# Performance work log

Hardware: AMD Instinct MI355X
Metric: run time of the kernel (lower is better)

## Reference

```python
import jax, jax.numpy as jnp
import numpy as np
from jax import lax

B, TZ, TT = 16, 2048, 512
D, DFF, L, V, HEADS = 256, 1024, 6, 512, 4
CH, HID, K, FLOWS, G = 256, 256, 5, 4, 256
PAD_ID = 0
NEG = -1e9
SCALE = 0.02


def setup_inputs():
    key = jax.random.key(0)
    ks = jax.random.split(key, 20)
    n = lambda i, shape, s=SCALE: jax.random.normal(ks[i], shape, jnp.float32) * s
    return {
        'z': jax.random.normal(ks[0], (B, TZ, CH), jnp.float32),
        'text': jax.random.randint(ks[1], (B, TT), 1, V),  # low=1 so no pad tokens
        'cond': jax.random.normal(ks[2], (B, G), jnp.float32),
        'embed': n(3, (V, D), 1.0),
        'wq': n(4, (L, D, D)), 'wk': n(5, (L, D, D)), 'wv': n(6, (L, D, D)), 'wo': n(7, (L, D, D)),
        'bq': jnp.zeros((L, D)), 'bk': jnp.zeros((L, D)), 'bv': jnp.zeros((L, D)), 'bo': jnp.zeros((L, D)),
        'ln1_g': jnp.ones((L, D)), 'ln1_b': jnp.zeros((L, D)),
        'ln2_g': jnp.ones((L, D)), 'ln2_b': jnp.zeros((L, D)),
        'w1': n(8, (L, D, DFF)), 'b1': jnp.zeros((L, DFF)),
        'w2': n(9, (L, DFF, D)), 'b2': jnp.zeros((L, D)),
        'mu_w': n(10, (D, D)), 'mu_b': jnp.zeros((D,)),
        'lv_w': n(11, (D, D)), 'lv_b': jnp.zeros((D,)),
        'flow_in': n(12, (FLOWS, CH // 2, HID)), 'flow_in_b': jnp.zeros((FLOWS, HID)),
        'flow_cond': n(13, (FLOWS, G, HID)),
        'flow_conv': n(14, (FLOWS, K, HID, HID)), 'flow_conv_b': jnp.zeros((FLOWS, HID)),
        'flow_out': n(15, (FLOWS, HID, CH // 2)), 'flow_out_b': jnp.zeros((FLOWS, CH // 2)),
    }


def _pos_encoding(length, d):
    pos = np.arange(length)[:, None].astype(np.float32)
    i = np.arange(d)[None, :]
    angle = pos / np.power(10000.0, (2 * (i // 2)) / d)
    pe = np.where(i % 2 == 0, np.sin(angle), np.cos(angle))
    return jnp.asarray(pe, jnp.float32)


def _ln(x, g, b):
    m = jnp.mean(x, -1, keepdims=True)
    v = jnp.var(x, -1, keepdims=True)
    return g * (x - m) * lax.rsqrt(v + 1e-6) + b


def _mha(x, wq, wk, wv, wo, bq, bk, bv, bo, bias):
    Bq, T, _ = x.shape
    dh = D // HEADS
    heads = lambda y: y.reshape(Bq, T, HEADS, dh).transpose(0, 2, 1, 3)
    q, k, v = heads(x @ wq + bq), heads(x @ wk + bk), heads(x @ wv + bv)
    scores = jnp.einsum('bhqd,bhkd->bhqk', q, k) / jnp.sqrt(jnp.float32(dh)) + bias
    attn = jax.nn.softmax(scores, axis=-1)
    out = jnp.einsum('bhqk,bhkd->bhqd', attn, v).transpose(0, 2, 1, 3).reshape(Bq, T, D)
    return out @ wo + bo


def _mas_path(logp, text_mask):
    # Viterbi monotonic alignment: each latent frame t maps to text index j(t),
    # j nondecreasing with steps in {0, 1}, start at 0, end at last valid token.
    Bq, Tz, Tt = logp.shape
    Q0 = jnp.where(jnp.arange(Tt) == 0, logp[:, 0, :], NEG)

    def fwd(Q, lt):
        Qs = jnp.concatenate([jnp.full((Bq, 1), NEG, Q.dtype), Q[:, :-1]], axis=1)
        return lt + jnp.maximum(Q, Qs), Qs > Q  # choice True => came from j-1

    _, choices = lax.scan(fwd, Q0, jnp.swapaxes(logp, 0, 1)[1:])  # [Tz-1,B,Tt]
    j_last = jnp.sum(text_mask, axis=1).astype(jnp.int32) - 1

    def bwd(j, ch):
        c = jnp.take_along_axis(ch, j[:, None], axis=1)[:, 0]
        jp = j - c.astype(jnp.int32)
        return jp, jp

    _, path_rev = lax.scan(bwd, j_last, choices[::-1])
    path = jnp.concatenate([path_rev[::-1], j_last[None]], axis=0)  # [Tz,B]
    return jnp.swapaxes(path, 0, 1)


def _forward(z, text, cond, embed, wq, wk, wv, wo, bq, bk, bv, bo, ln1_g, ln1_b, ln2_g, ln2_b,
             w1, b1, w2, b2, mu_w, mu_b, lv_w, lv_b,
             flow_in, flow_in_b, flow_cond, flow_conv, flow_conv_b, flow_out, flow_out_b):
    text_mask = text != PAD_ID  # [B,TT]
    bias = jnp.where(text_mask[:, None, None, :], 0.0, NEG)
    # text encoder: scaled embedding + sinusoidal PE + post-LN transformer blocks
    h = embed[text] * jnp.sqrt(jnp.float32(D)) + _pos_encoding(TT, D)[None]
    for l in range(L):
        h = _ln(h + _mha(h, wq[l], wk[l], wv[l], wo[l], bq[l], bk[l], bv[l], bo[l], bias), ln1_g[l], ln1_b[l])
        ffn = jax.nn.relu(h @ w1[l] + b1[l]) @ w2[l] + b2[l]
        h = _ln(h + ffn, ln2_g[l], ln2_b[l])
    mu = h @ mu_w + mu_b
    logvar = h @ lv_w + lv_b
    # residual coupling flows (mean-only, conditioned on global vector)
    zc = z
    for f in range(FLOWS):
        x0, x1 = jnp.split(zc, 2, axis=-1)
        hh = x0 @ flow_in[f] + flow_in_b[f] + (cond @ flow_cond[f])[:, None, :]
        hh = jnp.tanh(lax.conv_general_dilated(hh, flow_conv[f], (1,), 'SAME', rhs_dilation=(1,),
                                               dimension_numbers=('NWC', 'WIO', 'NWC')) + flow_conv_b[f])
        m = hh @ flow_out[f] + flow_out_b[f]
        zc = jnp.concatenate([x1 + m, x0], axis=-1)  # coupling + flip
    # gaussian log-likelihood between latent frames and text distributions
    spr = jnp.exp(-logvar)  # [B,TT,D]
    nc1 = jnp.sum(-0.5 * jnp.log(2.0 * jnp.pi) - 0.5 * logvar, axis=-1)  # [B,TT]
    nc2 = jnp.einsum('btd,bjd->btj', -0.5 * zc * zc, spr)
    nc3 = jnp.einsum('btd,bjd->btj', zc, mu * spr)
    nc4 = jnp.sum(-0.5 * mu * mu * spr, axis=-1)  # [B,TT]
    logp = nc1[:, None, :] + nc2 + nc3 + nc4[:, None, :]  # [B,TZ,TT]
    logp = jnp.where(text_mask[:, None, :], logp, NEG)
    path = _mas_path(logp, text_mask)  # [B,TZ] int32
    ctx = mu[jnp.arange(B)[:, None], path]  # expand text mu along latent time
    return ctx, h


def reference(z, text, cond, embed, wq, wk, wv, wo, bq, bk, bv, bo, ln1_g, ln1_b, ln2_g, ln2_b,
              w1, b1, w2, b2, mu_w, mu_b, lv_w, lv_b,
              flow_in, flow_in_b, flow_cond, flow_conv, flow_conv_b, flow_out, flow_out_b):
    return _forward(z, text, cond, embed, wq, wk, wv, wo, bq, bk, bv, bo, ln1_g, ln1_b, ln2_g, ln2_b,
                    w1, b1, w2, b2, mu_w, mu_b, lv_w, lv_b,
                    flow_in, flow_in_b, flow_cond, flow_conv, flow_conv_b, flow_out, flow_out_b)
```

## Files before the change

### kernel.cpp

```cpp
#include <hip/hip_runtime.h>

#define BB 16
#define TZ_ 2048
#define TT_ 512
#define D_ 256
#define DFF_ 1024
#define L_ 6
#define HEADS_ 4
#define DH_ 64
#define CH_ 256
#define HID_ 256
#define KCV 5
#define FLOWS_ 4
#define G_ 256
#define NEGF (-1000000000.0f)
#define LOG2PI 1.8378770664093453f

typedef unsigned short u16;
typedef __attribute__((ext_vector_type(8))) short short8v;
typedef __attribute__((ext_vector_type(4))) float f32x4;

__device__ __forceinline__ float wsum(float v){
#pragma unroll
  for (int o = 32; o; o >>= 1) v += __shfl_xor(v, o);
// ... 81 lines not shown
#pragma unroll
  for (int c=0;c<16;c+=4){
    float4 v = *(const float4*)(inb + (size_t)(kt + r)*istride + nt + cq + c);
    td[r][cq+c+0]=v.x; td[r][cq+c+1]=v.y; td[r][cq+c+2]=v.z; td[r][cq+c+3]=v.w;
  }
  __syncthreads();
#pragma unroll
  for (int c=0;c<16;c+=4){
    float4 v = make_float4(td[cq+c+0][r], td[cq+c+1][r], td[cq+c+2][r], td[cq+c+3][r]);
    *(float4*)(outb + (size_t)(nt + r)*ostride + kt + cq + c) = v;
  }
}

__global__ __launch_bounds__(256) void k_vt(const float* __restrict__ QKV, float* __restrict__ VT){
  __shared__ float td[64][65];
  const int b = blockIdx.z, dt = blockIdx.x, jt = blockIdx.y, t = threadIdx.x;
  const float* inb = QKV + (size_t)b*512*768 + 512;
  float* outb = VT + (size_t)b*131072;
  const int r = t>>2, cq = (t&3)*16;
#pragma unroll
  for (int c=0;c<16;c+=4){
    float4 v = *(const float4*)(inb + (size_t)(jt*64 + r)*768 + dt*64 + cq + c);
    td[r][cq+c+0]=v.x; td[r][cq+c+1]=v.y; td[r][cq+c+2]=v.z; td[r][cq+c+3]=v.w;
  }
  __syncthreads();
#pragma unroll
  for (int c=0;c<16;c+=4){
    float4 v = make_float4(td[cq+c+0][r], td[cq+c+1][r], td[cq+c+2][r], td[cq+c+3][r]);
    *(float4*)(outb + (size_t)(dt*64 + r)*512 + jt*64 + cq + c) = v;
  }
}

__global__ void k_bcat(const float* __restrict__ bq, const float* __restrict__ bk,
                       const float* __restrict__ bv, const float* __restrict__ mu_b,
                       const float* __restrict__ lv_b,
                       float* __restrict__ BQKV, float* __restrict__ MULVB){
  int i = blockIdx.x*256 + threadIdx.x;
  if (i < 4608){
    int l = i/768, c = i%768;
    float v = c<256 ? bq[l*256+c] : (c<512 ? bk[l*256+c-256] : bv[l*256+c-512]);
    BQKV[i] = v;
  } else if (i < 5120){
    int c = i-4608;
    MULVB[c] = c<256 ? mu_b[c] : lv_b[c-256];
  }
}

template<int WN, int EPI, int AM, int BMD>
__global__ __launch_bounds__(256,2) void k_mg(
  const void* __restrict__ Ap, const void* __restrict__ ApL, int lda, int azhi, int azlo,
  const void* __restrict__ Bp, const void* __restrict__ BpL, int ldb, int bzhi, int bzlo,
  const float* __restrict__ bias, const int* __restrict__ text,
  const float* __restrict__ nc1v, const float* __restrict__ nc4v,
  float* __restrict__ C, int ldc, int czhi, int czlo, int K)
{
  constexpr int BN = WN*32;
  __shared__ u16 AH[4096], AL[4096];
  __shared__ u16 BH[BN*32], BL[BN*32];
  char* AHB=(char*)AH; char* ALB=(char*)AL; char* BHB=(char*)BH; char* BLB=(char*)BL;
  const int t = threadIdx.x, z = blockIdx.z;
  const int m0 = blockIdx.y*128, n0 = blockIdx.x*BN;
  const size_t aoff = (size_t)(z>>2)*azhi + (size_t)(z&3)*azlo;
  const size_t boff = (size_t)(z>>2)*bzhi + (size_t)(z&3)*bzlo;
  const size_t coff = (size_t)(z>>2)*czhi + (size_t)(z&3)*czlo;
  const int w = t>>6, l = t&63;
  const int wr = (w>>1)*64, wc = (w&1)*(WN*16);
  const int lr = l&15, lg = l>>4;
  const int srow = t>>1, sseg = t&1;
  const int q  = (srow>>1)&3;
  const int wo0 = srow*64 + ((((sseg<<1)|0)^q)<<4);
  const int wo1 = srow*64 + ((((sseg<<1)|1)^q)<<4);
  const bool bact = (WN==4) || (t < 128);
  const int qa = ((wr+lr)>>1)&3, qb2 = ((wc+lr)>>1)&3;
  const int raBase = (wr+lr)*64 + ((lg^qa)<<4);
  const int rbBase = (wc+lr)*64 + ((lg^qb2)<<4);

  const float* Af = nullptr; const u16* AfH = nullptr; const u16* AfL = nullptr;
  if constexpr (AM==0 || AM==2){ Af = (const float*)Ap + aoff; }
  else { AfH = (const u16*)Ap + aoff; AfL = (const u16*)ApL + aoff; }
  const float* Bf = nullptr; const u16* BfH = nullptr; const u16* BfL = nullptr;
  if constexpr (BMD==0){ Bf = (const float*)Bp + boff; }
  else { BfH = (const u16*)Bp + boff; BfL = (const u16*)BpL + boff; }

  f32x4 acc[4][WN];
#pragma unroll
  for (int i=0;i<4;i++)
#pragma unroll
    for (int j=0;j<WN;j++) acc[i][j] = (f32x4){0.f,0.f,0.f,0.f};

  for (int k0 = 0; k0 < K; k0 += 32){
    uint4 ahi0, ahi1, alo0, alo1;
    if constexpr (AM==0){
      const float* p = Af + (size_t)(m0+srow)*lda + k0 + sseg*16;
      float4 a0=*(const float4*)p, a1=*(const float4*)(p+4);
      float4 a2=*(const float4*)(p+8), a3=*(const float4*)(p+12);
      cvt8t(a0,a1,ahi0,alo0); cvt8t(a2,a3,ahi1,alo1);
    } else if constexpr (AM==1){
      const u16* ph = AfH + (size_t)(m0+srow)*lda + k0 + sseg*16;
      const u16* pl = AfL + (size_t)(m0+srow)*lda + k0 + sseg*16;
      ahi0 = *(const uint4*)ph; ahi1 = *(const uint4*)(ph+8);
      alo0 = *(const uint4*)pl; alo1 = *(const uint4*)(pl+8);
    } else {
      int kg = k0 + sseg*16;
      const float* p = Af + (size_t)(m0+srow)*lda + (kg < 256 ? kg : kg - 256);
      float4 a0=*(const float4*)p, a1=*(const float4*)(p+4);
      float4 a2=*(const float4*)(p+8), a3=*(const float4*)(p+12);
      if (kg >= 256){
        a0.x=-0.5f*a0.x*a0.x; a0.y=-0.5f*a0.y*a0.y; a0.z=-0.5f*a0.z*a0.z; a0.w=-0.5f*a0.w*a0.w;
        a1.x=-0.5f*a1.x*a1.x; a1.y=-0.5f*a1.y*a1.y; a1.z=-0.5f*a1.z*a1.z; a1.w=-0.5f*a1.w*a1.w;
        a2.x=-0.5f*a2.x*a2.x; a2.y=-0.5f*a2.y*a2.y; a2.z=-0.5f*a2.z*a2.z; a2.w=-0.5f*a2.w*a2.w;
        a3.x=-0.5f*a3.x*a3.x; a3.y=-0.5f*a3.y*a3.y; a3.z=-0.5f*a3.z*a3.z; a3.w=-0.5f*a3.w*a3.w;
      }
      cvt8r(a0,a1,ahi0,alo0); cvt8r(a2,a3,ahi1,alo1);
    }
    uint4 bhi0, bhi1, blo0, blo1;
    if (bact){
      if constexpr (BMD==0){
        const float* p = Bf + (size_t)(n0+srow)*ldb + k0 + sseg*16;
        float4 b0=*(const float4*)p, b1=*(const float4*)(p+4);
        float4 b2=*(const float4*)(p+8), b3=*(const float4*)(p+12);
        cvt8t(b0,b1,bhi0,blo0); cvt8t(b2,b3,bhi1,blo1);
      } else {
        const u16* ph = BfH + (size_t)(n0+srow)*ldb + k0 + sseg*16;
        const u16* pl = BfL + (size_t)(n0+srow)*ldb + k0 + sseg*16;
        bhi0 = *(const uint4*)ph; bhi1 = *(const uint4*)(ph+8);
        blo0 = *(const uint4*)pl; blo1 = *(const uint4*)(pl+8);
      }
    }
    __syncthreads();
    *(uint4*)(AHB + wo0) = ahi0;  *(uint4*)(AHB + wo1) = ahi1;
    *(uint4*)(ALB + wo0) = alo0;  *(uint4*)(ALB + wo1) = alo1;
    if (bact){
      *(uint4*)(BHB + wo0) = bhi0;  *(uint4*)(BHB + wo1) = bhi1;
      *(uint4*)(BLB + wo0) = blo0;  *(uint4*)(BLB + wo1) = blo1;
    }
    __syncthreads();
    short8v fah[4], fal[4], fbh[WN], fbl[WN];
#pragma unroll
    for (int i=0;i<4;i++){
      fah[i] = *(short8v*)(AHB + raBase + i*1024);
      fal[i] = *(short8v*)(ALB + raBase + i*1024);
    }
#pragma unroll
    for (int j=0;j<WN;j++){
      fbh[j] = *(short8v*)(BHB + rbBase + j*1024);
      fbl[j] = *(short8v*)(BLB + rbBase + j*1024);
    }
#pragma unroll
    for (int i=0;i<4;i++)
#pragma unroll
      for (int j=0;j<WN;j++){
        acc[i][j] = __builtin_amdgcn_mfma_f32_16x16x32_bf16(fah[i], fbh[j], acc[i][j], 0,0,0);
        acc[i][j] = __builtin_amdgcn_mfma_f32_16x16x32_bf16(fal[i], fbh[j], acc[i][j], 0,0,0);
        acc[i][j] = __builtin_amdgcn_mfma_f32_16x16x32_bf16(fah[i], fbl[j], acc[i][j], 0,0,0);
      }
  }

#pragma unroll
  for (int i=0;i<4;i++){
    int mm0 = m0 + wr + i*16 + (lg<<2);
#pragma unroll
    for (int j=0;j<WN;j++){
      int nn = n0 + wc + j*16 + lr;
      float bs = 0.f; float ncb = 0.f; bool msk = true;
      if (EPI==0 || EPI==1) bs = bias ? bias[nn] : 0.f;
      if (EPI==2) msk = (text[(z>>2)*TT_ + nn] != 0);
      if (EPI==3){ ncb = nc1v[z*TT_+nn] + nc4v[z*TT_+nn]; msk = (text[z*TT_+nn] != 0); }
      f32x4 v = acc[i][j];
#pragma unroll
      for (int r=0;r<4;r++){
        int m = mm0 + r;
        float x;
        if (EPI==0)      x = v[r] + bs;
        else if (EPI==1) x = fmaxf(v[r] + bs, 0.f);
        else if (EPI==2) x = v[r]*0.125f + (msk ? 0.f : NEGF);
        else             x = msk ? (v[r] + ncb) : NEGF;
        C[coff + (size_t)m*ldc + nn] = x;
      }
    }
  }
}

__global__ __launch_bounds__(256) void k_softmax(float* __restrict__ S){
  size_t row = (size_t)blockIdx.x*4 + (threadIdx.x >> 6);
  float* p = S + row*TT_;
  int ln = threadIdx.x & 63;
  float4 a = *(float4*)(p + ln*8);
  float4 b = *(float4*)(p + ln*8 + 4);
  float x[8] = {a.x,a.y,a.z,a.w,b.x,b.y,b.z,b.w};
  float m = x[0];
#pragma unroll
  for (int i=1;i<8;i++) m = fmaxf(m, x[i]);
#pragma unroll
  for (int o2=32;o2;o2>>=1) m = fmaxf(m, __shfl_xor(m, o2));
  float s = 0.f;
#pragma unroll
  for (int i=0;i<8;i++){ x[i] = expf(x[i]-m); s += x[i]; }
  s = wsum(s);
  float inv = 1.0f/s;
  *(float4*)(p + ln*8)     = make_float4(x[0]*inv, x[1]*inv, x[2]*inv, x[3]*inv);
  *(float4*)(p + ln*8 + 4) = make_float4(x[4]*inv, x[5]*inv, x[6]*inv, x[7]*inv);
}

__global__ __launch_bounds__(256) void k_lnres(const float* __restrict__ y,
  const float* __restrict__ g, const float* __restrict__ bb, float* __restrict__ h){
  size_t row = blockIdx.x; int d = threadIdx.x;
  float v = h[row*D_ + d] + y[row*D_ + d];
  float s = wsum(v), s2 = wsum(v*v);
  __shared__ float r1[4], r2[4];
  int w = d >> 6;
  if ((d & 63) == 0){ r1[w] = s; r2[w] = s2; }
  __syncthreads();
  s  = r1[0]+r1[1]+r1[2]+r1[3];
  s2 = r2[0]+r2[1]+r2[2]+r2[3];
  float mean = s * (1.0f/D_);
  float var  = s2 * (1.0f/D_) - mean*mean;
  float inv  = rsqrtf(var + 1e-6f);
  h[row*D_ + d] = g[d]*(v - mean)*inv + bb[d];
// ... 38 lines not shown
    float wv2; u16 *dh, *dl; int idx;
    if (i < 32768){
      int n = i >> 7, k = i & 127;
      wv2 = win[k*256 + n]; dh = WITH; dl = WITL; idx = i;
    } else if (i < 360448){
      int jj = i - 32768;
      int o = jj / 1280, r = jj - o*1280;
      wv2 = wconv[(size_t)r*256 + o]; dh = WCTH; dl = WCTL; idx = jj;
    } else {
      int jj = i - 360448;
      int o = jj >> 8, k = jj & 255;
      wv2 = wout[k*128 + o]; dh = WOTH; dl = WOTL; idx = jj;
    }
    u16 hh = f2bf(wv2);
    dh[idx] = hh;
    dl[idx] = f2bf(wv2 - bf2f(hh));
  } else if (bid < 3584){
    size_t i = ((size_t)(bid-1536)*256 + t) << 3;
    size_t m2 = i >> 7; int k = (int)(i & 127);
    const float* src = zsrc + m2*256 + k;
    float4 a = *(const float4*)src; float4 b2 = *(const float4*)(src+4);
    float vv[8] = {a.x,a.y,a.z,a.w,b2.x,b2.y,b2.z,b2.w};
    short8v oh, ol;
#pragma unroll
    for (int r=0;r<8;r++){
      u16 hh = f2bf(vv[r]);
      oh[r] = (short)hh;
      ol[r] = (short)f2bf(vv[r] - bf2f(hh));
    }
    *(short8v*)(xh + i) = oh;
    *(short8v*)(xl + i) = ol;
  } else {
    int b = bid - 3584, n = t;
    float s = 0.f;
    for (int k2=0;k2<G_;k2++) s = fmaf(cond[b*G_ + k2], fcw[k2*HID_ + n], s);
    condp[b*HID_ + n] = s;
  }
}

__global__ void k_padzero2(u16* __restrict__ XpH, u16* __restrict__ XpL){
  int i = blockIdx.x*256 + threadIdx.x;
  u16* P = (i >> 14) ? XpL : XpH;
  int ii = i & 16383;
  int b = ii >> 10, rr = (ii >> 8) & 3, c = ii & 255;
  int row = (rr < 2) ? rr : (2048 + rr);
  P[((size_t)b*2052 + row)*256 + c] = 0;
}

template<int EPI, int SPLITOUT>
__global__ __launch_bounds__(256,2) void k_mf2(
  const u16* __restrict__ Ah, const u16* __restrict__ Al, int lda, int padA,
  const u16* __restrict__ Bh, const u16* __restrict__ Bl, int ldb,
  const float* __restrict__ bias, const float* __restrict__ cnd,
  void* __restrict__ CH, void* __restrict__ CL, int ldc, int padC, int K)
{
  __shared__ u16 AsmH[4096], AsmL[4096], BsmH[4096], BsmL[4096];
  char* AHB=(char*)AsmH; char* ALB=(char*)AsmL;
  char* BHB=(char*)BsmH; char* BLB=(char*)BsmL;
  const int t = threadIdx.x;
  const int m0 = blockIdx.y << 7, n0 = blockIdx.x << 7;
  const int w = t >> 6, l = t & 63;
  const int wr = (w >> 1) << 6, wc = (w & 1) << 6;
  const int lr = l & 15, lg = l >> 4;
  const int srow = t >> 1, sseg = t & 1;
  const int q = (srow >> 1) & 3;
  const int wo0 = srow*64 + ((((sseg<<1)|0) ^ q) << 4);
  const int wo1 = srow*64 + ((((sseg<<1)|1) ^ q) << 4);
  const int am = m0 + srow;
  const size_t aoff = (size_t)(am + padA*(am >> 11))*lda + (sseg << 4);
  const u16* AhP = Ah + aoff;
  const u16* AlP = Al + aoff;
  const size_t boff = (size_t)(n0 + srow)*ldb + (sseg << 4);
  const u16* BhP = Bh + boff;
  const u16* BlP = Bl + boff;
  const int qa = ((wr + lr) >> 1) & 3, qb = ((wc + lr) >> 1) & 3;
  const int raBase = (wr + lr)*64 + ((lg ^ qa) << 4);
  const int rbBase = (wc + lr)*64 + ((lg ^ qb) << 4);
  f32x4 acc[4][4];
#pragma unroll
  for (int i=0;i<4;i++)
#pragma unroll
    for (int j=0;j<4;j++) acc[i][j] = (f32x4){0.f,0.f,0.f,0.f};

  for (int k0 = 0; k0 < K; k0 += 32){
    float4 ah0 = *(const float4*)(AhP + k0);
    float4 ah1 = *(const float4*)(AhP + k0 + 8);
    float4 al0 = *(const float4*)(AlP + k0);
    float4 al1 = *(const float4*)(AlP + k0 + 8);
    float4 bh0 = *(const float4*)(BhP + k0);
    float4 bh1 = *(const float4*)(BhP + k0 + 8);
    float4 bl0 = *(const float4*)(BlP + k0);
    float4 bl1 = *(const float4*)(BlP + k0 + 8);
    __syncthreads();
    *(float4*)(AHB + wo0) = ah0;  *(float4*)(AHB + wo1) = ah1;
    *(float4*)(ALB + wo0) = al0;  *(float4*)(ALB + wo1) = al1;
    *(float4*)(BHB + wo0) = bh0;  *(float4*)(BHB + wo1) = bh1;
    *(float4*)(BLB + wo0) = bl0;  *(float4*)(BLB + wo1) = bl1;
    __syncthreads();
    short8v fah[4], fal[4], fbh[4], fbl[4];
#pragma unroll
    for (int i=0;i<4;i++){
      fah[i] = *(short8v*)(AHB + raBase + i*1024);
      fal[i] = *(short8v*)(ALB + raBase + i*1024);
    }
#pragma unroll
    for (int j=0;j<4;j++){
      fbh[j] = *(short8v*)(BHB + rbBase + j*1024);
      fbl[j] = *(short8v*)(BLB + rbBase + j*1024);
    }
#pragma unroll
    for (int i=0;i<4;i++)
#pragma unroll
      for (int j=0;j<4;j++){
        acc[i][j] = __builtin_amdgcn_mfma_f32_16x16x32_bf16(fah[i], fbh[j], acc[i][j], 0, 0, 0);
        acc[i][j] = __builtin_amdgcn_mfma_f32_16x16x32_bf16(fal[i], fbh[j], acc[i][j], 0, 0, 0);
        acc[i][j] = __builtin_amdgcn_mfma_f32_16x16x32_bf16(fah[i], fbl[j], acc[i][j], 0, 0, 0);
      }
  }

#pragma unroll
  for (int i=0;i<4;i++){
    int mbase = m0 + wr + i*16 + (lg << 2);
#pragma unroll
    for (int j=0;j<4;j++){
      int nn = n0 + wc + j*16 + lr;
      float bs = bias[nn];
      f32x4 v = acc[i][j];
#pragma unroll
      for (int r=0;r<4;r++){
        int m = mbase + r;
        float x = v[r] + bs;
        if (EPI == 1) x += cnd[((m >> 11) << 8) + nn];
        if (EPI == 2) x = tanhf(x);
        if (EPI == 3) x += cnd[(size_t)m*256 + 128 + nn];
        size_t ro = (size_t)(m + padC*(m >> 11))*ldc + nn;
        if (SPLITOUT){
          u16 xh = f2bf(x);
          ((u16*)CH)[ro] = xh;
          ((u16*)CL)[ro] = f2bf(x - bf2f(xh));
        } else {
          ((float*)CH)[ro] = x;
          if (EPI == 3)
            ((float*)CH)[(size_t)m*ldc + 128 + nn] = cnd[(size_t)m*256 + nn];
        }
      }
    }
  }
}

#define MCH 8
#define NCHK (TZ_/MCH)
__device__ __forceinline__ int swsl(int s){ return s ^ ((s>>3)&7); }

__device__ __forceinline__ void mas_row(float4 u0, float4 u1, float* Q, int ln, int tr,
                                        unsigned char* __restrict__ cb){
  if (tr == 0){
    if (ln == 0) Q[0] = u0.x;
    return;
  }
  float v[8] = {u0.x,u0.y,u0.z,u0.w,u1.x,u1.y,u1.z,u1.w};
  float qp = __shfl_up(Q[7], 1);
  if (ln == 0) qp = NEGF;
  unsigned bits = 0; float qs = qp;
#pragma unroll
  for (int i=0;i<8;i++){
    float old = Q[i];
    if (qs > old) bits |= (1u<<i);
    Q[i] = v[i] + fmaxf(old, qs);
    qs = old;
  }
  cb[(size_t)(tr-1)*64 + ln] = (unsigned char)bits;
}

__global__ __launch_bounds__(512) void k_mas(const float* __restrict__ lp,
  const int* __restrict__ text, unsigned char* __restrict__ cho, int* __restrict__ path)
{
  const int b = blockIdx.x, t = threadIdx.x, ln = t & 63;
  const float* L = lp + (size_t)b*TZ_*TT_;
  __shared__ float buf[3][MCH*TT_];
  __shared__ __align__(16) unsigned char lch[3][4096];
  const int frow = t >> 6, k64 = t & 63;
  const size_t gsrc = (size_t)frow*TT_ + k64*8;
  char* b0p = (char*)&buf[0][0];
  char* b1p = (char*)&buf[1][0];
  char* b2p = (char*)&buf[2][0];
  char* bufb[3] = {b0p, b1p, b2p};
  const int wroff = frow*2048;
  const int ws0 = wroff + (swsl(2*k64)<<4);
  const int ws1 = wroff + (swsl(2*k64+1)<<4);
  const int rs0 = swsl(2*ln)<<4;
  const int rs1 = swsl(2*ln+1)<<4;
  unsigned char* cb = cho + (size_t)b*TZ_*64;

  {
    float4 a0 = *(const float4*)(L + gsrc);
    float4 a1 = *(const float4*)(L + gsrc + 4);
    float4 c0 = *(const float4*)(L + (size_t)MCH*TT_ + gsrc);
    float4 c1 = *(const float4*)(L + (size_t)MCH*TT_ + gsrc + 4);
    *(float4*)(b0p + ws0) = a0;  *(float4*)(b0p + ws1) = a1;
    *(float4*)(b1p + ws0) = c0;  *(float4*)(b1p + ws1) = c1;
  }
  float4 pA0 = *(const float4*)(L + (size_t)2*MCH*TT_ + gsrc);
  float4 pA1 = *(const float4*)(L + (size_t)2*MCH*TT_ + gsrc + 4);
  float4 pB0 = *(const float4*)(L + (size_t)3*MCH*TT_ + gsrc);
  float4 pB1 = *(const float4*)(L + (size_t)3*MCH*TT_ + gsrc + 4);
  __syncthreads();

  float Q[8];
#pragma unroll
  for (int i=0;i<8;i++) Q[i] = NEGF;
  float4 hA0,hA1,hA2,hA3,hA4,hA5,hA6,hA7;
  float4 hB0,hB1,hB2,hB3,hB4,hB5,hB6,hB7;
  if (t < 64){
    hA0 = *(float4*)(b0p + 0*2048 + rs0); hA1 = *(float4*)(b0p + 0*2048 + rs1);
    hA2 = *(float4*)(b0p + 1*2048 + rs0); hA3 = *(float4*)(b0p + 1*2048 + rs1);
    hA4 = *(float4*)(b0p + 2*2048 + rs0); hA5 = *(float4*)(b0p + 2*2048 + rs1);
    hA6 = *(float4*)(b0p + 3*2048 + rs0); hA7 = *(float4*)(b0p + 3*2048 + rs1);
  }
  int cur = 0;
  for (int ch = 0; ch < NCHK; ch++){
    if (ch + 2 < NCHK){
      char* wb = bufb[(cur+2)%3];
      if (ch & 1){ *(float4*)(wb + ws0) = pB0; *(float4*)(wb + ws1) = pB1; }
      else       { *(float4*)(wb + ws0) = pA0; *(float4*)(wb + ws1) = pA1; }
    }
    if (ch + 4 < NCHK){
      const float* src = L + (size_t)(ch+4)*MCH*TT_ + gsrc;
      if (ch & 1){ pB0 = *(const float4*)src; pB1 = *(const float4*)(src+4); }
      else       { pA0 = *(const float4*)src; pA1 = *(const float4*)(src+4); }
    }
    if (t < 64){
      char* cbuf = bufb[cur];
      char* nbuf = bufb[(cur+1)%3];
      hB0 = *(float4*)(cbuf + 4*2048 + rs0); hB1 = *(float4*)(cbuf + 4*2048 + rs1);
      hB2 = *(float4*)(cbuf + 5*2048 + rs0); hB3 = *(float4*)(cbuf + 5*2048 + rs1);
      hB4 = *(float4*)(cbuf + 6*2048 + rs0); hB5 = *(float4*)(cbuf + 6*2048 + rs1);
      hB6 = *(float4*)(cbuf + 7*2048 + rs0); hB7 = *(float4*)(cbuf + 7*2048 + rs1);
      mas_row(hA0,hA1,Q,ln, ch*MCH+0, cb);
      mas_row(hA2,hA3,Q,ln, ch*MCH+1, cb);
      mas_row(hA4,hA5,Q,ln, ch*MCH+2, cb);
      mas_row(hA6,hA7,Q,ln, ch*MCH+3, cb);
      hA0 = *(float4*)(nbuf + 0*2048 + rs0); hA1 = *(float4*)(nbuf + 0*2048 + rs1);
      hA2 = *(float4*)(nbuf + 1*2048 + rs0); hA3 = *(float4*)(nbuf + 1*2048 + rs1);
      hA4 = *(float4*)(nbuf + 2*2048 + rs0); hA5 = *(float4*)(nbuf + 2*2048 + rs1);
      hA6 = *(float4*)(nbuf + 3*2048 + rs0); hA7 = *(float4*)(nbuf + 3*2048 + rs1);
      mas_row(hB0,hB1,Q,ln, ch*MCH+4, cb);
      mas_row(hB2,hB3,Q,ln, ch*MCH+5, cb);
      mas_row(hB4,hB5,Q,ln, ch*MCH+6, cb);
      mas_row(hB6,hB7,Q,ln, ch*MCH+7, cb);
    }
    __syncthreads();
    cur++; if (cur >= 3) cur = 0;
  }

  int jl = 0;
  if (t < 64){
    int cnt = 0;
#pragma unroll
    for (int i=0;i<8;i++) cnt += (text[b*TT_ + ln*8 + i] != 0) ? 1 : 0;
#pragma unroll
    for (int o2=32;o2;o2>>=1) cnt += __shfl_xor(cnt, o2);
    jl = cnt - 1;
  }
  if (t == 0) path[b*TZ_ + TZ_-1] = jl;
  __syncthreads();

  const int NP = TZ_ - 1;
  const int NH = 32;
  uint* lchU0 = (uint*)&lch[0][0];
  uint* lchU1 = (uint*)&lch[1][0];
  uint* lchU2 = (uint*)&lch[2][0];
  uint* lchU[3] = {lchU0, lchU1, lchU2};
  const uint* cbU = (const uint*)cb;
  {
#pragma unroll
    for (int k=0;k<2;k++){
      int d = t + k*512;
      int p = (d >> 4);
      lchU0[d] = cbU[(size_t)(2046 - p)*16 + (d & 15)];
      lchU1[d] = cbU[(size_t)(2046 - (64 + p))*16 + (d & 15)];
    }
  }
  uint uA0, uA1, uB0, uB1;
  {
    int d0 = t, d1 = t + 512;
    uA0 = cbU[(size_t)(2046 - (128 + (d0>>4)))*16 + (d0 & 15)];
    uA1 = cbU[(size_t)(2046 - (128 + (d1>>4)))*16 + (d1 & 15)];
    uB0 = cbU[(size_t)(2046 - (192 + (d0>>4)))*16 + (d0 & 15)];
    uB1 = cbU[(size_t)(2046 - (192 + (d1>>4)))*16 + (d1 & 15)];
  }
  __syncthreads();

  int j = jl;
  unsigned rb0[8], rb1[8]; int rc[8];
  if (t == 0){
#pragma unroll
    for (int qd=0; qd<8; qd++){
      int cHi = jl >> 3;
      int cLo = (cHi > 0) ? cHi - 1 : 0;
      rb1[qd] = lch[0][(qd)*64 + cHi];
      rb0[qd] = lch[0][(qd)*64 + cLo];
      rc[qd]  = cHi;
    }
  }
  for (int H = 0; H < NH; H++){
    if (H + 2 < NH){
      uint* wb = lchU[(H+2)%3];
      if (H & 1){ wb[t] = uB0; wb[t+512] = uB1; }
      else      { wb[t] = uA0; wb[t+512] = uA1; }
    }
    if (H + 4 < NH){
      int d0 = t, d1 = t + 512;
      int base = (H+4)*64;
      int p0 = base + (d0>>4), p1 = base + (d1>>4);
      uint v0 = (p0 <= 2046) ? cbU[(size_t)(2046 - p0)*16 + (d0 & 15)] : 0u;
      uint v1 = (p1 <= 2046) ? cbU[(size_t)(2046 - p1)*16 + (d1 & 15)] : 0u;
      if (H & 1){ uB0 = v0; uB1 = v1; }
      else      { uA0 = v0; uA1 = v1; }
    }
    if (t == 0){
      int pbase = H*64;
#pragma unroll 8
      for (int s = 0; s < 64; s++){
        int p = pbase + s;
        if (p < NP){
          int r = s & 7;
          int jb = j >> 3;
          unsigned byte = (jb == rc[r]) ? rb1[r] : rb0[r];
          j -= (int)((byte >> (j & 7)) & 1u);
          path[b*TZ_ + 2046 - p] = j;
          int pn = p + 8;
          if (pn < NP){
            int hn = (pn >> 6) % 3, sn = pn & 63;
            int cHi = j >> 3;
            int cLo = (cHi > 0) ? cHi - 1 : 0;
            rb1[r] = lch[hn][sn*64 + cHi];
            rb0[r] = lch[hn][sn*64 + cLo];
            rc[r]  = cHi;
          }
        }
      }
    }
    __syncthreads();
  }
}

__global__ void k_gather(const float* __restrict__ mulv, const int* __restrict__ path,
  const float* __restrict__ h, float* __restrict__ out){
  size_t i = (size_t)blockIdx.x*256 + threadIdx.x;
  const size_t N4 = (size_t)BB*TZ_*(D_/4);
  const size_t H4 = (size_t)BB*TT_*(D_/4);
  if (i < N4){
    size_t row = i >> 6; int c = (int)(i & 63);
    int b = (int)(row >> 11);
    int pj = path[row];
    ((float4*)out)[i] = *(const float4*)(mulv + ((size_t)b*TT_ + pj)*512 + (size_t)c*4);
  } else if (i < N4 + H4){
    size_t k2 = i - N4;
    ((float4*)out)[i] = ((const float4*)h)[k2];
  }
}

extern "C" void kernel_launch(void* const* d_in, const int* in_sizes, int n_in,
                              void* d_out, int out_size, void* d_ws, size_t ws_size,
                              hipStream_t stream)
{
  (void)in_sizes; (void)n_in; (void)out_size; (void)ws_size;
  const float* z      = (const float*)d_in[0];
  const int*   text   = (const int*)  d_in[1];
  const float* cond   = (const float*)d_in[2];
  const float* emb    = (const float*)d_in[3];
  const float* wq     = (const float*)d_in[4];
  const float* wk     = (const float*)d_in[5];
  const float* wv     = (const float*)d_in[6];
  const float* wo     = (const float*)d_in[7];
  const float* bq     = (const float*)d_in[8];
  const float* bk     = (const float*)d_in[9];
  const float* bv     = (const float*)d_in[10];
  const float* bo     = (const float*)d_in[11];
  const float* ln1g   = (const float*)d_in[12];
  const float* ln1b   = (const float*)d_in[13];
  const float* ln2g   = (const float*)d_in[14];
  const float* ln2b   = (const float*)d_in[15];
  const float* w1     = (const float*)d_in[16];
  const float* b1     = (const float*)d_in[17];
  const float* w2     = (const float*)d_in[18];
  const float* b2     = (const float*)d_in[19];
  const float* mu_w   = (const float*)d_in[20];
  const float* mu_b   = (const float*)d_in[21];
  const float* lv_w   = (const float*)d_in[22];
  const float* lv_b   = (const float*)d_in[23];
  const float* f_in   = (const float*)d_in[24];
  const float* f_in_b = (const float*)d_in[25];
  const float* f_cond = (const float*)d_in[26];
  const float* f_conv = (const float*)d_in[27];
  const float* f_convb= (const float*)d_in[28];
  const float* f_out  = (const float*)d_in[29];
  const float* f_outb = (const float*)d_in[30];

  float* ws = (float*)d_ws;
  size_t o = 0;
  float* PE   = ws + o; o += (size_t)131072;
  float* H    = ws + o; o += (size_t)2097152;
  float* MULV = ws + o; o += (size_t)4194304;
  float* NC1  = ws + o; o += (size_t)8192;
  float* NC4  = ws + o; o += (size_t)8192;
  float* CONDP= ws + o; o += (size_t)4096;
  int*   PATH = (int*)(ws + o); o += (size_t)32768;
  u16*  B2H  = (u16*)(ws + o); o += (size_t)2097152;
  u16*  B2L  = (u16*)(ws + o); o += (size_t)2097152;
  float* BIGS = ws + o; o += (size_t)16777216;
  float* BUF1 = ws + o; o += (size_t)4587520;
  float* BUF2 = ws + o; o += (size_t)10485760;
  float* ZCA  = ws + o; o += (size_t)8388608;
  float* ZCB  = ws + o; o += (size_t)8388608;

  float* QKV = BUF2;
  float* Yb  = QKV + 6291456;
  float* VT  = Yb + 2097152;
  float* ATTO= QKV;
// ... 84 lines not shown
```

Baseline: 2.685 ms.

## Prefetch next K-tile in GEMM loops and unswizzle MAS shared buffers

Both GEMM kernels now load the next K-slice from global memory into registers while the current slice is written to LDS and consumed by MFMAs, giving register-level double buffering that hides global load latency. This costs extra live registers and could lower occupancy. The MAS kernel's LDS buffers are also flattened and the XOR swizzle on the staging layout is dropped in favour of a linear layout. The unswizzled layout may change LDS bank-conflict behaviour on the per-row reads.

Result: faster. 2.320 ms (-13.6%).

```diff
diff --git a/kernel.cpp b/kernel.cpp
--- a/kernel.cpp
+++ b/kernel.cpp
@@ -187,29 +187,49 @@
   if constexpr (BMD==0){ Bf = (const float*)Bp + boff; }
   else { BfH = (const u16*)Bp + boff; BfL = (const u16*)BpL + boff; }
 
-  f32x4 acc[4][WN];
-#pragma unroll
-  for (int i=0;i<4;i++)
-#pragma unroll
-    for (int j=0;j<WN;j++) acc[i][j] = (f32x4){0.f,0.f,0.f,0.f};
-
-  for (int k0 = 0; k0 < K; k0 += 32){
+  float4 sa0, sa1, sa2, sa3;
+  uint4  pah0, pah1, pal0, pal1;
+  float4 sb0, sb1, sb2, sb3;
+  uint4  pbh0, pbh1, pbl0, pbl1;
+
+  auto LOADA = [&](int kk){
+    if constexpr (AM==0){
+      const float* p = Af + (size_t)(m0+srow)*lda + kk + sseg*16;
+      sa0=*(const float4*)p; sa1=*(const float4*)(p+4);
+      sa2=*(const float4*)(p+8); sa3=*(const float4*)(p+12);
+    } else if constexpr (AM==1){
+      const u16* ph = AfH + (size_t)(m0+srow)*lda + kk + sseg*16;
+      const u16* pl = AfL + (size_t)(m0+srow)*lda + kk + sseg*16;
+      pah0 = *(const uint4*)ph; pah1 = *(const uint4*)(ph+8);
+      pal0 = *(const uint4*)pl; pal1 = *(const uint4*)(pl+8);
+    } else {
+      int kg = kk + sseg*16;
+      const float* p = Af + (size_t)(m0+srow)*lda + (kg < 256 ? kg : kg - 256);
+      sa0=*(const float4*)p; sa1=*(const float4*)(p+4);
+      sa2=*(const float4*)(p+8); sa3=*(const float4*)(p+12);
+    }
+  };
+  auto LOADB = [&](int kk){
+    if constexpr (BMD==0){
+      const float* p = Bf + (size_t)(n0+srow)*ldb + kk + sseg*16;
+      sb0=*(const float4*)p; sb1=*(const float4*)(p+4);
+      sb2=*(const float4*)(p+8); sb3=*(const float4*)(p+12);
+    } else {
+      const u16* ph = BfH + (size_t)(n0+srow)*ldb + kk + sseg*16;
+      const u16* pl = BfL + (size_t)(n0+srow)*ldb + kk + sseg*16;
+      pbh0 = *(const uint4*)ph; pbh1 = *(const uint4*)(ph+8);
+      pbl0 = *(const uint4*)pl; pbl1 = *(const uint4*)(pl+8);
+    }
+  };
+  auto WRITEA = [&](int kk){
     uint4 ahi0, ahi1, alo0, alo1;
     if constexpr (AM==0){
-      const float* p = Af + (size_t)(m0+srow)*lda + k0 + sseg*16;
-      float4 a0=*(const float4*)p, a1=*(const float4*)(p+4);
-      float4 a2=*(const float4*)(p+8), a3=*(const float4*)(p+12);
-      cvt8t(a0,a1,ahi0,alo0); cvt8t(a2,a3,ahi1,alo1);
+      cvt8t(sa0,sa1,ahi0,alo0); cvt8t(sa2,sa3,ahi1,alo1);
     } else if constexpr (AM==1){
-      const u16* ph = AfH + (size_t)(m0+srow)*lda + k0 + sseg*16;
-      const u16* pl = AfL + (size_t)(m0+srow)*lda + k0 + sseg*16;
-      ahi0 = *(const uint4*)ph; ahi1 = *(const uint4*)(ph+8);
-      alo0 = *(const uint4*)pl; alo1 = *(const uint4*)(pl+8);
+      ahi0=pah0; ahi1=pah1; alo0=pal0; alo1=pal1;
     } else {
-      int kg = k0 + sseg*16;
-      const float* p = Af + (size_t)(m0+srow)*lda + (kg < 256 ? kg : kg - 256);
-      float4 a0=*(const float4*)p, a1=*(const float4*)(p+4);
-      float4 a2=*(const float4*)(p+8), a3=*(const float4*)(p+12);
+      float4 a0=sa0, a1=sa1, a2=sa2, a3=sa3;
+      int kg = kk + sseg*16;
       if (kg >= 256){
         a0.x=-0.5f*a0.x*a0.x; a0.y=-0.5f*a0.y*a0.y; a0.z=-0.5f*a0.z*a0.z; a0.w=-0.5f*a0.w*a0.w;
         a1.x=-0.5f*a1.x*a1.x; a1.y=-0.5f*a1.y*a1.y; a1.z=-0.5f*a1.z*a1.z; a1.w=-0.5f*a1.w*a1.w;
@@ -218,27 +238,33 @@
       }
       cvt8r(a0,a1,ahi0,alo0); cvt8r(a2,a3,ahi1,alo1);
     }
-    uint4 bhi0, bhi1, blo0, blo1;
-    if (bact){
-      if constexpr (BMD==0){
-        const float* p = Bf + (size_t)(n0+srow)*ldb + k0 + sseg*16;
-        float4 b0=*(const float4*)p, b1=*(const float4*)(p+4);
-        float4 b2=*(const float4*)(p+8), b3=*(const float4*)(p+12);
-        cvt8t(b0,b1,bhi0,blo0); cvt8t(b2,b3,bhi1,blo1);
-      } else {
-        const u16* ph = BfH + (size_t)(n0+srow)*ldb + k0 + sseg*16;
-        const u16* pl = BfL + (size_t)(n0+srow)*ldb + k0 + sseg*16;
-        bhi0 = *(const uint4*)ph; bhi1 = *(const uint4*)(ph+8);
-        blo0 = *(const uint4*)pl; blo1 = *(const uint4*)(pl+8);
-      }
-    }
-    __syncthreads();
     *(uint4*)(AHB + wo0) = ahi0;  *(uint4*)(AHB + wo1) = ahi1;
     *(uint4*)(ALB + wo0) = alo0;  *(uint4*)(ALB + wo1) = alo1;
-    if (bact){
-      *(uint4*)(BHB + wo0) = bhi0;  *(uint4*)(BHB + wo1) = bhi1;
-      *(uint4*)(BLB + wo0) = blo0;  *(uint4*)(BLB + wo1) = blo1;
-    }
+  };
+  auto WRITEB = [&](){
+    uint4 bhi0, bhi1, blo0, blo1;
+    if constexpr (BMD==0){
+      cvt8t(sb0,sb1,bhi0,blo0); cvt8t(sb2,sb3,bhi1,blo1);
+    } else {
+      bhi0=pbh0; bhi1=pbh1; blo0=pbl0; blo1=pbl1;
+    }
+    *(uint4*)(BHB + wo0) = bhi0;  *(uint4*)(BHB + wo1) = bhi1;
+    *(uint4*)(BLB + wo0) = blo0;  *(uint4*)(BLB + wo1) = blo1;
+  };
+
+  f32x4 acc[4][WN];
+#pragma unroll
+  for (int i=0;i<4;i++)
+#pragma unroll
+    for (int j=0;j<WN;j++) acc[i][j] = (f32x4){0.f,0.f,0.f,0.f};
+
+  LOADA(0);
+  if (bact) LOADB(0);
+  for (int k0 = 0; k0 < K; k0 += 32){
+    __syncthreads();
+    WRITEA(k0);
+    if (bact) WRITEB();
+    if (k0 + 32 < K){ LOADA(k0+32); if (bact) LOADB(k0+32); }
     __syncthreads();
     short8v fah[4], fal[4], fbh[WN], fbl[WN];
 #pragma unroll
@@ -443,20 +469,22 @@
 #pragma unroll
     for (int j=0;j<4;j++) acc[i][j] = (f32x4){0.f,0.f,0.f,0.f};
 
+  float4 sah0, sah1, sal0, sal1, sbh0, sbh1, sbl0, sbl1;
+  auto LOADF = [&](int kk){
+    sah0 = *(const float4*)(AhP + kk); sah1 = *(const float4*)(AhP + kk + 8);
+    sal0 = *(const float4*)(AlP + kk); sal1 = *(const float4*)(AlP + kk + 8);
+    sbh0 = *(const float4*)(BhP + kk); sbh1 = *(const float4*)(BhP + kk + 8);
+    sbl0 = *(const float4*)(BlP + kk); sbl1 = *(const float4*)(BlP + kk + 8);
+  };
+
+  LOADF(0);
   for (int k0 = 0; k0 < K; k0 += 32){
-    float4 ah0 = *(const float4*)(AhP + k0);
-    float4 ah1 = *(const float4*)(AhP + k0 + 8);
-    float4 al0 = *(const float4*)(AlP + k0);
-    float4 al1 = *(const float4*)(AlP + k0 + 8);
-    float4 bh0 = *(const float4*)(BhP + k0);
-    float4 bh1 = *(const float4*)(BhP + k0 + 8);
-    float4 bl0 = *(const float4*)(BlP + k0);
-    float4 bl1 = *(const float4*)(BlP + k0 + 8);
     __syncthreads();
-    *(float4*)(AHB + wo0) = ah0;  *(float4*)(AHB + wo1) = ah1;
-    *(float4*)(ALB + wo0) = al0;  *(float4*)(ALB + wo1) = al1;
-    *(float4*)(BHB + wo0) = bh0;  *(float4*)(BHB + wo1) = bh1;
-    *(float4*)(BLB + wo0) = bl0;  *(float4*)(BLB + wo1) = bl1;
+    *(float4*)(AHB + wo0) = sah0;  *(float4*)(AHB + wo1) = sah1;
+    *(float4*)(ALB + wo0) = sal0;  *(float4*)(ALB + wo1) = sal1;
+    *(float4*)(BHB + wo0) = sbh0;  *(float4*)(BHB + wo1) = sbh1;
+    *(float4*)(BLB + wo0) = sbl0;  *(float4*)(BLB + wo1) = sbl1;
+    if (k0 + 32 < K) LOADF(k0 + 32);
     __syncthreads();
     short8v fah[4], fal[4], fbh[4], fbl[4];
 #pragma unroll
@@ -511,7 +539,6 @@
 
 #define MCH 8
 #define NCHK (TZ_/MCH)
-__device__ __forceinline__ int swsl(int s){ return s ^ ((s>>3)&7); }
 
 __device__ __forceinline__ void mas_row(float4 u0, float4 u1, float* Q, int ln, int tr,
                                         unsigned char* __restrict__ cb){
@@ -538,19 +565,12 @@
 {
   const int b = blockIdx.x, t = threadIdx.x, ln = t & 63;
   const float* L = lp + (size_t)b*TZ_*TT_;
-  __shared__ float buf[3][MCH*TT_];
-  __shared__ __align__(16) unsigned char lch[3][4096];
-  const int frow = t >> 6, k64 = t & 63;
-  const size_t gsrc = (size_t)frow*TT_ + k64*8;
-  char* b0p = (char*)&buf[0][0];
-  char* b1p = (char*)&buf[1][0];
-  char* b2p = (char*)&buf[2][0];
-  char* bufb[3] = {b0p, b1p, b2p};
-  const int wroff = frow*2048;
-  const int ws0 = wroff + (swsl(2*k64)<<4);
-  const int ws1 = wroff + (swsl(2*k64+1)<<4);
-  const int rs0 = swsl(2*ln)<<4;
-  const int rs1 = swsl(2*ln+1)<<4;
+  __shared__ float buf[3*MCH*TT_];
+  __shared__ __align__(16) unsigned char lch[3*4096];
+  const int frow = t >> 6, lc = t & 63;
+  const size_t gsrc = (size_t)frow*TT_ + lc*8;
+  char* base = (char*)&buf[0];
+  const int wrB = frow*2048 + lc*16;
   unsigned char* cb = cho + (size_t)b*TZ_*64;
 
   {
@@ -558,8 +578,10 @@
     float4 a1 = *(const float4*)(L + gsrc + 4);
     float4 c0 = *(const float4*)(L + (size_t)MCH*TT_ + gsrc);
     float4 c1 = *(const float4*)(L + (size_t)MCH*TT_ + gsrc + 4);
-    *(float4*)(b0p + ws0) = a0;  *(float4*)(b0p + ws1) = a1;
-    *(float4*)(b1p + ws0) = c0;  *(float4*)(b1p + ws1) = c1;
+    *(float4*)(base + 0*16384 + wrB)        = a0;
+    *(float4*)(base + 0*16384 + wrB + 1024) = a1;
+    *(float4*)(base + 1*16384 + wrB)        = c0;
+    *(float4*)(base + 1*16384 + wrB + 1024) = c1;
   }
   float4 pA0 = *(const float4*)(L + (size_t)2*MCH*TT_ + gsrc);
   float4 pA1 = *(const float4*)(L + (size_t)2*MCH*TT_ + gsrc + 4);
@@ -570,20 +592,22 @@
   float Q[8];
 #pragma unroll
   for (int i=0;i<8;i++) Q[i] = NEGF;
+  const int rB = ln*16;
   float4 hA0,hA1,hA2,hA3,hA4,hA5,hA6,hA7;
   float4 hB0,hB1,hB2,hB3,hB4,hB5,hB6,hB7;
   if (t < 64){
-    hA0 = *(float4*)(b0p + 0*2048 + rs0); hA1 = *(float4*)(b0p + 0*2048 + rs1);
-    hA2 = *(float4*)(b0p + 1*2048 + rs0); hA3 = *(float4*)(b0p + 1*2048 + rs1);
-    hA4 = *(float4*)(b0p + 2*2048 + rs0); hA5 = *(float4*)(b0p + 2*2048 + rs1);
-    hA6 = *(float4*)(b0p + 3*2048 + rs0); hA7 = *(float4*)(b0p + 3*2048 + rs1);
+    hA0 = *(float4*)(base + 0*2048 + rB); hA1 = *(float4*)(base + 0*2048 + rB + 1024);
+    hA2 = *(float4*)(base + 1*2048 + rB); hA3 = *(float4*)(base + 1*2048 + rB + 1024);
+    hA4 = *(float4*)(base + 2*2048 + rB); hA5 = *(float4*)(base + 2*2048 + rB + 1024);
+    hA6 = *(float4*)(base + 3*2048 + rB); hA7 = *(float4*)(base + 3*2048 + rB + 1024);
   }
   int cur = 0;
   for (int ch = 0; ch < NCHK; ch++){
+    int wIdx = cur + 2; if (wIdx >= 3) wIdx -= 3;
     if (ch + 2 < NCHK){
-      char* wb = bufb[(cur+2)%3];
-      if (ch & 1){ *(float4*)(wb + ws0) = pB0; *(float4*)(wb + ws1) = pB1; }
-      else       { *(float4*)(wb + ws0) = pA0; *(float4*)(wb + ws1) = pA1; }
+      char* wb = base + wIdx*16384;
+      if (ch & 1){ *(float4*)(wb + wrB) = pB0; *(float4*)(wb + wrB + 1024) = pB1; }
+      else       { *(float4*)(wb + wrB) = pA0; *(float4*)(wb + wrB + 1024) = pA1; }
     }
     if (ch + 4 < NCHK){
       const float* src = L + (size_t)(ch+4)*MCH*TT_ + gsrc;
@@ -591,20 +615,21 @@
       else       { pA0 = *(const float4*)src; pA1 = *(const float4*)(src+4); }
     }
     if (t < 64){
-      char* cbuf = bufb[cur];
-      char* nbuf = bufb[(cur+1)%3];
-      hB0 = *(float4*)(cbuf + 4*2048 + rs0); hB1 = *(float4*)(cbuf + 4*2048 + rs1);
-      hB2 = *(float4*)(cbuf + 5*2048 + rs0); hB3 = *(float4*)(cbuf + 5*2048 + rs1);
-      hB4 = *(float4*)(cbuf + 6*2048 + rs0); hB5 = *(float4*)(cbuf + 6*2048 + rs1);
-      hB6 = *(float4*)(cbuf + 7*2048 + rs0); hB7 = *(float4*)(cbuf + 7*2048 + rs1);
+      char* cbuf = base + cur*16384;
+      int nIdx = cur + 1; if (nIdx >= 3) nIdx -= 3;
+      char* nbuf = base + nIdx*16384;
+      hB0 = *(float4*)(cbuf + 4*2048 + rB); hB1 = *(float4*)(cbuf + 4*2048 + rB + 1024);
+      hB2 = *(float4*)(cbuf + 5*2048 + rB); hB3 = *(float4*)(cbuf + 5*2048 + rB + 1024);
+      hB4 = *(float4*)(cbuf + 6*2048 + rB); hB5 = *(float4*)(cbuf + 6*2048 + rB + 1024);
+      hB6 = *(float4*)(cbuf + 7*2048 + rB); hB7 = *(float4*)(cbuf + 7*2048 + rB + 1024);
       mas_row(hA0,hA1,Q,ln, ch*MCH+0, cb);
       mas_row(hA2,hA3,Q,ln, ch*MCH+1, cb);
       mas_row(hA4,hA5,Q,ln, ch*MCH+2, cb);
       mas_row(hA6,hA7,Q,ln, ch*MCH+3, cb);
-      hA0 = *(float4*)(nbuf + 0*2048 + rs0); hA1 = *(float4*)(nbuf + 0*2048 + rs1);
-      hA2 = *(float4*)(nbuf + 1*2048 + rs0); hA3 = *(float4*)(nbuf + 1*2048 + rs1);
-      hA4 = *(float4*)(nbuf + 2*2048 + rs0); hA5 = *(float4*)(nbuf + 2*2048 + rs1);
-      hA6 = *(float4*)(nbuf + 3*2048 + rs0); hA7 = *(float4*)(nbuf + 3*2048 + rs1);
+      hA0 = *(float4*)(nbuf + 0*2048 + rB); hA1 = *(float4*)(nbuf + 0*2048 + rB + 1024);
+      hA2 = *(float4*)(nbuf + 1*2048 + rB); hA3 = *(float4*)(nbuf + 1*2048 + rB + 1024);
+      hA4 = *(float4*)(nbuf + 2*2048 + rB); hA5 = *(float4*)(nbuf + 2*2048 + rB + 1024);
+      hA6 = *(float4*)(nbuf + 3*2048 + rB); hA7 = *(float4*)(nbuf + 3*2048 + rB + 1024);
       mas_row(hB0,hB1,Q,ln, ch*MCH+4, cb);
       mas_row(hB2,hB3,Q,ln, ch*MCH+5, cb);
       mas_row(hB4,hB5,Q,ln, ch*MCH+6, cb);
@@ -628,18 +653,15 @@
 
   const int NP = TZ_ - 1;
   const int NH = 32;
-  uint* lchU0 = (uint*)&lch[0][0];
-  uint* lchU1 = (uint*)&lch[1][0];
-  uint* lchU2 = (uint*)&lch[2][0];
-  uint* lchU[3] = {lchU0, lchU1, lchU2};
+  uint* lchU = (uint*)lch;
   const uint* cbU = (const uint*)cb;
   {
 #pragma unroll
-    for (int k=0;k<2;k++){
+    for (int k = 0; k < 2; k++){
       int d = t + k*512;
-      int p = (d >> 4);
-      lchU0[d] = cbU[(size_t)(2046 - p)*16 + (d & 15)];
-      lchU1[d] = cbU[(size_t)(2046 - (64 + p))*16 + (d & 15)];
+      int p = d >> 4;
+      lchU[d]        = cbU[(size_t)(2046 - p)*16 + (d & 15)];
+      lchU[1024 + d] = cbU[(size_t)(2046 - (64 + p))*16 + (d & 15)];
     }
   }
   uint uA0, uA1, uB0, uB1;
@@ -659,21 +681,22 @@
     for (int qd=0; qd<8; qd++){
       int cHi = jl >> 3;
       int cLo = (cHi > 0) ? cHi - 1 : 0;
-      rb1[qd] = lch[0][(qd)*64 + cHi];
-      rb0[qd] = lch[0][(qd)*64 + cLo];
+      rb1[qd] = lch[qd*64 + cHi];
+      rb0[qd] = lch[qd*64 + cLo];
       rc[qd]  = cHi;
     }
   }
   for (int H = 0; H < NH; H++){
     if (H + 2 < NH){
-      uint* wb = lchU[(H+2)%3];
+      int wslot = (H + 2) % 3;
+      uint* wb = lchU + wslot*1024;
       if (H & 1){ wb[t] = uB0; wb[t+512] = uB1; }
       else      { wb[t] = uA0; wb[t+512] = uA1; }
     }
     if (H + 4 < NH){
       int d0 = t, d1 = t + 512;
-      int base = (H+4)*64;
-      int p0 = base + (d0>>4), p1 = base + (d1>>4);
+      int bse = (H+4)*64;
+      int p0 = bse + (d0>>4), p1 = bse + (d1>>4);
       uint v0 = (p0 <= 2046) ? cbU[(size_t)(2046 - p0)*16 + (d0 & 15)] : 0u;
       uint v1 = (p1 <= 2046) ? cbU[(size_t)(2046 - p1)*16 + (d1 & 15)] : 0u;
       if (H & 1){ uB0 = v0; uB1 = v1; }
@@ -695,8 +718,8 @@
             int hn = (pn >> 6) % 3, sn = pn & 63;
             int cHi = j >> 3;
             int cLo = (cHi > 0) ? cHi - 1 : 0;
-            rb1[r] = lch[hn][sn*64 + cHi];
-            rb0[r] = lch[hn][sn*64 + cLo];
+            rb1[r] = lch[hn*4096 + sn*64 + cHi];
+            rb0[r] = lch[hn*4096 + sn*64 + cLo];
             rc[r]  = cHi;
           }
         }
```
